# Optimization experiments

Hardware: AMD Instinct MI355X
Metric: run time of the kernel (lower is better)

Reference implementation:

```python
import jax, jax.numpy as jnp
import numpy as np

N_NODES = 50000
N_EDGES = 1600000
N_GRAPHS = 256
IN_CH = 128
HID = 128
OUT_CH = 10


def gcn_conv(x, W, b, src, dst, ew, num_nodes):
    # PyG GCNConv: add self-loops (weight 1), symmetric deg^-1/2 normalization,
    # linear transform first, aggregate via scatter-add, bias after.
    loop = jnp.arange(num_nodes)
    s = jnp.concatenate([src, loop])
    d = jnp.concatenate([dst, loop])
    w = jnp.concatenate([ew, jnp.ones((num_nodes,), x.dtype)])
    deg = jax.ops.segment_sum(w, d, num_segments=num_nodes)
    dinv = jnp.where(deg > 0, jax.lax.rsqrt(deg), 0.0)
    norm = dinv[s] * dinv[d] * w                     # [E+N]
    h = x @ W                                        # [N, H]
    msg = h[s] * norm[:, None]                       # gather + scale
    out = jax.ops.segment_sum(msg, d, num_segments=num_nodes)  # scatter-add
    return out + b


def setup_inputs() -> dict:
    key = jax.random.key(0)
    ks = jax.random.split(key, 12)
    x = jax.random.normal(ks[0], (N_NODES, IN_CH), jnp.float32)
    edge_index = jax.random.randint(ks[1], (2, N_EDGES), 0, N_NODES, jnp.int64)
    edge_weight = jax.random.uniform(ks[2], (N_EDGES,), jnp.float32)
    batch = jnp.sort(jax.random.randint(ks[3], (N_NODES,), 0, N_GRAPHS, jnp.int64))
    s = 1.0 / np.sqrt(HID)
    W1 = jax.random.normal(ks[4], (IN_CH, HID), jnp.float32) / np.sqrt(IN_CH)
    b1 = jnp.zeros((HID,), jnp.float32)
    W2 = jax.random.normal(ks[5], (HID, HID), jnp.float32) * s
    b2 = jnp.zeros((HID,), jnp.float32)
    W3 = jax.random.normal(ks[6], (HID, HID), jnp.float32) * s
    b3 = jnp.zeros((HID,), jnp.float32)
    lw1 = jax.random.normal(ks[7], (HID, HID), jnp.float32) * s
    lb1 = jax.random.normal(ks[8], (HID,), jnp.float32) * s
    lw2 = jax.random.normal(ks[9], (HID, OUT_CH), jnp.float32) * s
    lb2 = jax.random.normal(ks[10], (OUT_CH,), jnp.float32) * s
    return {"x": x, "edge_index": edge_index, "edge_weight": edge_weight,
            "batch": batch, "W1": W1, "b1": b1, "W2": W2, "b2": b2,
            "W3": W3, "b3": b3, "lw1": lw1, "lb1": lb1, "lw2": lw2, "lb2": lb2}


def reference(x, edge_index, edge_weight, batch, W1, b1, W2, b2, W3, b3, lw1, lb1, lw2, lb2):
    src, dst = edge_index[0], edge_index[1]
    h = jax.nn.relu(gcn_conv(x, W1, b1, src, dst, edge_weight, N_NODES))
    h = jax.nn.relu(gcn_conv(h, W2, b2, src, dst, edge_weight, N_NODES))
    h = gcn_conv(h, W3, b3, src, dst, edge_weight, N_NODES)
    # global mean pool over graphs
    sums = jax.ops.segment_sum(h, batch, num_segments=N_GRAPHS)
    cnt = jax.ops.segment_sum(jnp.ones((N_NODES,), h.dtype), batch, num_segments=N_GRAPHS)
    emb = sums / jnp.maximum(cnt, 1.0)[:, None]      # [G, HID]
    out = (emb @ lw1 + lb1) @ lw2 + lb2              # classify: lin1 -> lin2
    return out
```

## Files before the change

### kernel.cpp

```cpp
#include <hip/hip_runtime.h>

#define N_NODES 50000
#define N_EDGES 1600000
#define N_GRAPHS 256
#define HID 128
#define OUT_CH 10
#define NBUCK 512
#define BNODES ((N_NODES + NBUCK - 1) / NBUCK)
#define BCAP 6144
#define P1BLK 250
#define EPB (N_EDGES / P1BLK)
#define DSENTINEL 127
#define NR 4
#define RSTEP ((N_NODES + NR - 1) / NR)
#define PAD_R 40

typedef __bf16 bf16x8 __attribute__((ext_vector_type(8)));
typedef float f32x4 __attribute__((ext_vector_type(4)));

__device__ inline unsigned bf16rne(float f) {
    unsigned u = __float_as_uint(f);
    return (u + 0x7fffu + ((u >> 16) & 1u)) >> 16;
}

__global__ __launch_bounds__(1024) void bucket_k(const int* __restrict__ src,
                                                 const int* __restrict__ dst,
                                                 const float* __restrict__ ew,
                                                 int* __restrict__ bcount,
                                                 int2* __restrict__ cpair) {
    __shared__ int hist[NBUCK];
    __shared__ int base[NBUCK];
    int t = threadIdx.x;
    for (int i = t; i < NBUCK; i += 1024) hist[i] = 0;
    __syncthreads();
    const int ch0 = blockIdx.x * (EPB / 4);
    const int ch1 = ch0 + (EPB / 4);
    const int4* dst4 = (const int4*)dst;
    for (int ci = ch0 + t; ci < ch1; ci += 1024) {
        int4 d4 = dst4[ci];
        atomicAdd(&hist[d4.x / BNODES], 1);
        atomicAdd(&hist[d4.y / BNODES], 1);
        atomicAdd(&hist[d4.z / BNODES], 1);
        atomicAdd(&hist[d4.w / BNODES], 1);
    }
    __syncthreads();
    for (int i = t; i < NBUCK; i += 1024) {
        int c = hist[i];
        base[i] = (c > 0) ? atomicAdd(&bcount[i], (c + 7) & ~7) : 0;
        hist[i] = 0;
    }
    __syncthreads();
    for (int ci = ch0 + t; ci < ch1; ci += 1024) {
        int4 d4 = dst4[ci];
        int e = ci * 4;
#define PROC(dd, ee)                                              \
        {                                                         \
            int b = (dd) / BNODES;                                \
            int off = base[b] + atomicAdd(&hist[b], 1);           \
            if (off < BCAP) {                                     \
                int2 p;                                           \
                p.x = (((dd) - b * BNODES) << 16) | src[ee];      \
                p.y = __float_as_int(ew[ee]);                     \
                cpair[b * BCAP + off] = p;                        \
            }                                                     \
        }
        PROC(d4.x, e)
        PROC(d4.y, e + 1)
        PROC(d4.z, e + 2)
        PROC(d4.w, e + 3)
#undef PROC
    }
    __syncthreads();
    for (int i = t; i < NBUCK; i += 1024) {
        int c = hist[i];
        int ac = (c + 7) & ~7;
        for (int j = c; j < ac; ++j) {
            int off = base[i] + j;
            if (off < BCAP) {
                int2 p;
                p.x = DSENTINEL << 16;
                p.y = 0;
                cpair[i * BCAP + off] = p;
            }
        }
    }
}

__global__ __launch_bounds__(512) void ell_scatter_k(const int* __restrict__ bcount,
                                                     const int2* __restrict__ cpair,
                                                     int2* __restrict__ ell,
                                                     unsigned* __restrict__ fill4,
                                                     float* __restrict__ dinv) {
    __shared__ int lfill[BNODES * NR];
    __shared__ float wsum[BNODES];
    int b = blockIdx.x;
    int t = threadIdx.x;
    for (int i = t; i < BNODES * NR; i += 512) lfill[i] = 0;
    for (int i = t; i < BNODES; i += 512) wsum[i] = 0.f;
    __syncthreads();
    int cnt = bcount[b];
    if (cnt > BCAP) cnt = BCAP;
    int n0 = b * BNODES;
    int sbase = b * BCAP;
    for (int i = t; i < cnt; i += 512) {
        int2 p = cpair[sbase + i];
        int dloc = p.x >> 16;
        if (dloc < BNODES) {
            int s = p.x & 0xffff;
            int r = s / RSTEP;
            int pos = atomicAdd(&lfill[dloc * NR + r], 1);
            atomicAdd(&wsum[dloc], __int_as_float(p.y));
            if (pos < PAD_R) {
                int2 q;
                q.x = s;
                q.y = p.y;
                ell[((size_t)(n0 + dloc) * NR + r) * PAD_R + pos] = q;
            }
        }
    }
    __syncthreads();
    for (int i = t; i < BNODES; i += 512) {
        int n = n0 + i;
        if (n < N_NODES) {
            unsigned f = 0;
#pragma unroll
            for (int r = 0; r < NR; ++r) {
                int c = lfill[i * NR + r];
                if (c > PAD_R) c = PAD_R;
                f |= (unsigned)c << (8 * r);
            }
            fill4[n] = f;
            dinv[n] = rsqrtf(wsum[i] + 1.0f);
        }
    }
}

__global__ __launch_bounds__(256) void prep_k(const int* __restrict__ batch,
                                              int* __restrict__ gstart,
                                              const float* __restrict__ W1,
                                              const float* __restrict__ W2,
                                              const float* __restrict__ W3,
                                              unsigned short* __restrict__ Wt) {
    int idx = blockIdx.x * 256 + threadIdx.x;
    if (idx < 3 * 16384) {
        int m = idx >> 14;
        int r = idx & 16383;
        const float* W = (m == 0) ? W1 : (m == 1) ? W2 : W3;
        int c = r >> 7, k = r & 127;
        Wt[idx] = (unsigned short)bf16rne(W[k * 128 + c]);
    }
    if (idx < N_NODES) {
        int b = batch[idx];
        int bprev = (idx == 0) ? -1 : batch[idx - 1];
        for (int g = bprev + 1; g <= b; ++g) gstart[g] = idx;
        if (idx == N_NODES - 1) {
            for (int g = b + 1; g <= N_GRAPHS; ++g) gstart[g] = N_NODES;
        }
    }
}

__global__ __launch_bounds__(256) void gemm_mfma_k(const float* __restrict__ A32,
                                                   const unsigned short* __restrict__ Ab,
                                                   const unsigned short* __restrict__ Wt,
                                                   unsigned short* __restrict__ Cb,
                                                   int n_rows) {
    int tid = threadIdx.x;
    int wave = tid >> 6;
    int lane = tid & 63;
    int m = lane & 15;
    int quad = lane >> 4;
    int row = blockIdx.x * 64 + wave * 16 + m;
    int rowc = row < n_rows ? row : n_rows - 1;
    f32x4 acc[8] = {};
#pragma unroll
    for (int kc = 0; kc < 4; ++kc) {
        bf16x8 a;
        if (A32) {
            const float4* Ar = (const float4*)(A32 + (size_t)rowc * 128 + kc * 32 + quad * 8);
            float4 lo = Ar[0], hi = Ar[1];
            union { bf16x8 v; unsigned short s[8]; } u;
            u.s[0] = (unsigned short)bf16rne(lo.x);
            u.s[1] = (unsigned short)bf16rne(lo.y);
            u.s[2] = (unsigned short)bf16rne(lo.z);
            u.s[3] = (unsigned short)bf16rne(lo.w);
            u.s[4] = (unsigned short)bf16rne(hi.x);
            u.s[5] = (unsigned short)bf16rne(hi.y);
            u.s[6] = (unsigned short)bf16rne(hi.z);
            u.s[7] = (unsigned short)bf16rne(hi.w);
            a = u.v;
        } else {
            a = *(const bf16x8*)(Ab + (size_t)rowc * 128 + kc * 32 + quad * 8);
        }
#pragma unroll
        for (int ct = 0; ct < 8; ++ct) {
            bf16x8 b = *(const bf16x8*)(Wt + (size_t)(ct * 16 + m) * 128 + kc * 32 + quad * 8);
            acc[ct] = __builtin_amdgcn_mfma_f32_16x16x32_bf16(a, b, acc[ct], 0, 0, 0);
        }
    }
    int obase = blockIdx.x * 64 + wave * 16 + quad * 4;
#pragma unroll
    for (int ct = 0; ct < 8; ++ct) {
#pragma unroll
        for (int r = 0; r < 4; ++r) {
            int n = obase + r;
            if (n < n_rows)
                Cb[(size_t)n * 128 + ct * 16 + m] = (unsigned short)bf16rne(acc[ct][r]);
        }
    }
}

__global__ __launch_bounds__(256) void agg_k(const unsigned short* __restrict__ tb,
                                             const unsigned* __restrict__ fill4,
                                             const int2* __restrict__ ell,
                                             const float* __restrict__ dinv,
                                             const float* __restrict__ bias,
                                             unsigned short* __restrict__ outB, int relu) {
    int lane = threadIdx.x & 15;
    int local = threadIdx.x >> 4;
    int n = blockIdx.x * 16 + local;
    if (n >= N_NODES) return;
    float dn = dinv[n];
#define UNP(q, f)                                                 \
    float f##0 = __uint_as_float((q).x << 16);                    \
    float f##1 = __uint_as_float((q).x & 0xffff0000u);            \
    float f##2 = __uint_as_float((q).y << 16);                    \
    float f##3 = __uint_as_float((q).y & 0xffff0000u);            \
    float f##4 = __uint_as_float((q).z << 16);                    \
    float f##5 = __uint_as_float((q).z & 0xffff0000u);            \
    float f##6 = __uint_as_float((q).w << 16);                    \
    float f##7 = __uint_as_float((q).w & 0xffff0000u);
    uint4 qs = ((const uint4*)(tb + (size_t)n * 128))[lane];
    UNP(qs, s)
    float acc0 = s0 * dn, acc1 = s1 * dn, acc2 = s2 * dn, acc3 = s3 * dn;
    float acc4 = s4 * dn, acc5 = s5 * dn, acc6 = s6 * dn, acc7 = s7 * dn;
    unsigned f4 = fill4[n];
#pragma unroll
    for (int r = 0; r < NR; ++r) {
        int c = (f4 >> (8 * r)) & 255;
        const int2* ep = ell + ((size_t)n * NR + r) * PAD_R;
        int i = 0;
        for (; i + 4 <= c; i += 4) {
            int2 p0 = ep[i], p1 = ep[i + 1], p2 = ep[i + 2], p3 = ep[i + 3];
            uint4 q0 = ((const uint4*)(tb + (size_t)p0.x * 128))[lane];
            uint4 q1 = ((const uint4*)(tb + (size_t)p1.x * 128))[lane];
            uint4 q2 = ((const uint4*)(tb + (size_t)p2.x * 128))[lane];
            uint4 q3 = ((const uint4*)(tb + (size_t)p3.x * 128))[lane];
            float w0 = __int_as_float(p0.y) * dinv[p0.x];
            float w1 = __int_as_float(p1.y) * dinv[p1.x];
            float w2 = __int_as_float(p2.y) * dinv[p2.x];
            float w3 = __int_as_float(p3.y) * dinv[p3.x];
            UNP(q0, a)
            UNP(q1, b)
            UNP(q2, cc)
            UNP(q3, d)
            acc0 += a0 * w0 + b0 * w1 + cc0 * w2 + d0 * w3;
            acc1 += a1 * w0 + b1 * w1 + cc1 * w2 + d1 * w3;
            acc2 += a2 * w0 + b2 * w1 + cc2 * w2 + d2 * w3;
            acc3 += a3 * w0 + b3 * w1 + cc3 * w2 + d3 * w3;
            acc4 += a4 * w0 + b4 * w1 + cc4 * w2 + d4 * w3;
            acc5 += a5 * w0 + b5 * w1 + cc5 * w2 + d5 * w3;
            acc6 += a6 * w0 + b6 * w1 + cc6 * w2 + d6 * w3;
            acc7 += a7 * w0 + b7 * w1 + cc7 * w2 + d7 * w3;
        }
        for (; i < c; ++i) {
            int2 p = ep[i];
            float w = __int_as_float(p.y) * dinv[p.x];
            uint4 q = ((const uint4*)(tb + (size_t)p.x * 128))[lane];
            UNP(q, a)
            acc0 += a0 * w; acc1 += a1 * w; acc2 += a2 * w; acc3 += a3 * w;
            acc4 += a4 * w; acc5 += a5 * w; acc6 += a6 * w; acc7 += a7 * w;
        }
    }
#undef UNP
    float4 b0 = ((const float4*)bias)[lane * 2];
    float4 b1 = ((const float4*)bias)[lane * 2 + 1];
    acc0 = acc0 * dn + b0.x; acc1 = acc1 * dn + b0.y;
    acc2 = acc2 * dn + b0.z; acc3 = acc3 * dn + b0.w;
    acc4 = acc4 * dn + b1.x; acc5 = acc5 * dn + b1.y;
    acc6 = acc6 * dn + b1.z; acc7 = acc7 * dn + b1.w;
    if (relu) {
        acc0 = fmaxf(acc0, 0.f); acc1 = fmaxf(acc1, 0.f);
        acc2 = fmaxf(acc2, 0.f); acc3 = fmaxf(acc3, 0.f);
        acc4 = fmaxf(acc4, 0.f); acc5 = fmaxf(acc5, 0.f);
        acc6 = fmaxf(acc6, 0.f); acc7 = fmaxf(acc7, 0.f);
    }
    uint4 pk;
    pk.x = bf16rne(acc0) | (bf16rne(acc1) << 16);
    pk.y = bf16rne(acc2) | (bf16rne(acc3) << 16);
    pk.z = bf16rne(acc4) | (bf16rne(acc5) << 16);
    pk.w = bf16rne(acc6) | (bf16rne(acc7) << 16);
    ((uint4*)(outB + (size_t)n * 128))[lane] = pk;
}

#define PCHUNK 49
__global__ __launch_bounds__(128) void pool1_k(const unsigned short* __restrict__ hb,
                                               const int* __restrict__ batch,
                                               float* __restrict__ pool) {
    int c = threadIdx.x;
    int n0 = blockIdx.x * PCHUNK;
    if (n0 >= N_NODES) return;
    int n1 = n0 + PCHUNK;
    if (n1 > N_NODES) n1 = N_NODES;
    int g = batch[n0];
    float run = 0.f;
    for (int n = n0; n < n1; ++n) {
        int gn = batch[n];
        if (gn != g) {
            atomicAdd(&pool[g * 128 + c], run);
            run = 0.f;
            g = gn;
        }
        run += __uint_as_float((unsigned)hb[(size_t)n * 128 + c] << 16);
    }
    atomicAdd(&pool[g * 128 + c], run);
}

__global__ __launch_bounds__(128) void cls2_k(const float* __restrict__ pool,
                                              const int* __restrict__ gstart,
                                              const float* __restrict__ lw1,
                                              const float* __restrict__ lb1,
                                              const float* __restrict__ lw2,
                                              const float* __restrict__ lb2,
                                              float* __restrict__ out) {
    __shared__ float emb[128];
    __shared__ float mid[128];
    int g = blockIdx.x, c = threadIdx.x;
    float cntf = fmaxf((float)(gstart[g + 1] - gstart[g]), 1.0f);
    emb[c] = pool[(size_t)g * 128 + c] / cntf;
    __syncthreads();
    float a = lb1[c];
    for (int k = 0; k < 128; ++k) a += emb[k] * lw1[k * 128 + c];
    mid[c] = a;
    __syncthreads();
    if (c < OUT_CH) {
        float o = lb2[c];
        for (int k = 0; k < 128; ++k) o += mid[k] * lw2[k * OUT_CH + c];
        out[g * OUT_CH + c] = o;
    }
}

extern "C" void kernel_launch(void* const* d_in, const int* in_sizes, int n_in,
                              void* d_out, int out_size, void* d_ws, size_t ws_size,
                              hipStream_t stream) {
    const float* x = (const float*)d_in[0];
    const int* ei = (const int*)d_in[1];
    const int* src = ei;
    const int* dst = ei + N_EDGES;
    const float* ew = (const float*)d_in[2];
    const int* batch = (const int*)d_in[3];
    const float* W1 = (const float*)d_in[4];
    const float* b1 = (const float*)d_in[5];
    const float* W2 = (const float*)d_in[6];
    const float* b2 = (const float*)d_in[7];
    const float* W3 = (const float*)d_in[8];
    const float* b3 = (const float*)d_in[9];
    const float* lw1 = (const float*)d_in[10];
    const float* lb1 = (const float*)d_in[11];
    const float* lw2 = (const float*)d_in[12];
    const float* lb2 = (const float*)d_in[13];
    float* out = (float*)d_out;

    char* ws = (char*)d_ws;
    size_t off = 0;
    auto alloc = [&](size_t bytes) {
        size_t cur = off;
        off += (bytes + 255) & ~(size_t)255;
        return cur;
    };
    size_t o_bcount = alloc(NBUCK * 4);
    size_t o_pool = alloc(N_GRAPHS * HID * 4);
    size_t zero_end = off;
    size_t o_fill4 = alloc(N_NODES * 4);
    size_t o_dinv = alloc(N_NODES * 4);
    size_t o_gstart = alloc((N_GRAPHS + 1) * 4);
    size_t o_wt = alloc(3 * 16384 * 2);
    size_t o_ell = alloc((size_t)N_NODES * NR * PAD_R * 8);
    size_t o_cpair = alloc((size_t)NBUCK * BCAP * 8);
    size_t o_gAb = alloc((size_t)N_NODES * HID * 2);
    size_t o_aggB = alloc((size_t)N_NODES * HID * 2);
    (void)ws_size;

    int* bcount = (int*)(ws + o_bcount);
    float* pool = (float*)(ws + o_pool);
    unsigned* fill4 = (unsigned*)(ws + o_fill4);
    float* dinv = (float*)(ws + o_dinv);
    int* gstart = (int*)(ws + o_gstart);
    unsigned short* Wt = (unsigned short*)(ws + o_wt);
    int2* ell = (int2*)(ws + o_ell);
    int2* cpair = (int2*)(ws + o_cpair);
    unsigned short* gAb = (unsigned short*)(ws + o_gAb);
    unsigned short* aggB = (unsigned short*)(ws + o_aggB);

    hipMemsetAsync(d_ws, 0, zero_end, stream);

    bucket_k<<<P1BLK, 1024, 0, stream>>>(src, dst, ew, bcount, cpair);
    ell_scatter_k<<<NBUCK, 512, 0, stream>>>(bcount, cpair, ell, fill4, dinv);
    prep_k<<<196, 256, 0, stream>>>(batch, gstart, W1, W2, W3, Wt);

    int gemm_blocks = (N_NODES + 63) / 64;
    int agg_blocks = (N_NODES + 15) / 16;
    gemm_mfma_k<<<gemm_blocks, 256, 0, stream>>>(x, (const unsigned short*)0, Wt, gAb, N_NODES);
    agg_k<<<agg_blocks, 256, 0, stream>>>(gAb, fill4, ell, dinv, b1, aggB, 1);
    gemm_mfma_k<<<gemm_blocks, 256, 0, stream>>>((const float*)0, aggB, Wt + 16384, gAb, N_NODES);
    agg_k<<<agg_blocks, 256, 0, stream>>>(gAb, fill4, ell, dinv, b2, aggB, 1);
    gemm_mfma_k<<<gemm_blocks, 256, 0, stream>>>((const float*)0, aggB, Wt + 32768, gAb, N_NODES);
    agg_k<<<agg_blocks, 256, 0, stream>>>(gAb, fill4, ell, dinv, b3, aggB, 0);

    pool1_k<<<(N_NODES + PCHUNK - 1) / PCHUNK, 128, 0, stream>>>(aggB, batch, pool);
    cls2_k<<<N_GRAPHS, 128, 0, stream>>>(pool, gstart, lw1, lb1, lw2, lb2, out);
}
```

Measured before the change: 385.7 us.

## Merge four per-range ELL slots into one contiguous row-sorted ELL row

The ELL build now makes two passes per bucket. The first counts edges per source range and sums weights, then per-node prefix offsets are computed so all of a node's edges sit in one contiguous PAD=80 row, still grouped by source range. The aggregation kernel then walks a single list per node, not four short sub-lists, which cuts loop overhead and remainder iterations and lets the 4-way unroll cover more edges. Separately, the bucket kernel loads src and edge weights as vectors. The cost is a second pass over the bucketed pairs, and any node with more than 80 in-edges would be truncated.

Measured after the change: 389.9 us. No clear change (+1.1%).

```diff
diff --git a/kernel.cpp b/kernel.cpp
--- a/kernel.cpp
+++ b/kernel.cpp
@@ -5,6 +5,7 @@
 #define N_GRAPHS 256
 #define HID 128
 #define OUT_CH 10
+#define PAD 80
 #define NBUCK 512
 #define BNODES ((N_NODES + NBUCK - 1) / NBUCK)
 #define BCAP 6144
@@ -13,7 +14,6 @@
 #define DSENTINEL 127
 #define NR 4
 #define RSTEP ((N_NODES + NR - 1) / NR)
-#define PAD_R 40
 
 typedef __bf16 bf16x8 __attribute__((ext_vector_type(8)));
 typedef float f32x4 __attribute__((ext_vector_type(4)));
@@ -36,6 +36,8 @@
     const int ch0 = blockIdx.x * (EPB / 4);
     const int ch1 = ch0 + (EPB / 4);
     const int4* dst4 = (const int4*)dst;
+    const int4* src4 = (const int4*)src;
+    const float4* ew4 = (const float4*)ew;
     for (int ci = ch0 + t; ci < ch1; ci += 1024) {
         int4 d4 = dst4[ci];
         atomicAdd(&hist[d4.x / BNODES], 1);
@@ -52,22 +54,23 @@
     __syncthreads();
     for (int ci = ch0 + t; ci < ch1; ci += 1024) {
         int4 d4 = dst4[ci];
-        int e = ci * 4;
-#define PROC(dd, ee)                                              \
+        int4 s4 = src4[ci];
+        float4 w4 = ew4[ci];
+#define PROC(dd, ss, ww)                                          \
         {                                                         \
             int b = (dd) / BNODES;                                \
             int off = base[b] + atomicAdd(&hist[b], 1);           \
             if (off < BCAP) {                                     \
                 int2 p;                                           \
-                p.x = (((dd) - b * BNODES) << 16) | src[ee];      \
-                p.y = __float_as_int(ew[ee]);                     \
+                p.x = (((dd) - b * BNODES) << 16) | (ss);         \
+                p.y = __float_as_int(ww);                         \
                 cpair[b * BCAP + off] = p;                        \
             }                                                     \
         }
-        PROC(d4.x, e)
-        PROC(d4.y, e + 1)
-        PROC(d4.z, e + 2)
-        PROC(d4.w, e + 3)
+        PROC(d4.x, s4.x, w4.x)
+        PROC(d4.y, s4.y, w4.y)
+        PROC(d4.z, s4.z, w4.z)
+        PROC(d4.w, s4.w, w4.w)
 #undef PROC
     }
     __syncthreads();
@@ -89,13 +92,13 @@
 __global__ __launch_bounds__(512) void ell_scatter_k(const int* __restrict__ bcount,
                                                      const int2* __restrict__ cpair,
                                                      int2* __restrict__ ell,
-                                                     unsigned* __restrict__ fill4,
+                                                     int* __restrict__ fill,
                                                      float* __restrict__ dinv) {
-    __shared__ int lfill[BNODES * NR];
+    __shared__ int lcnt[BNODES * NR];
     __shared__ float wsum[BNODES];
     int b = blockIdx.x;
     int t = threadIdx.x;
-    for (int i = t; i < BNODES * NR; i += 512) lfill[i] = 0;
+    for (int i = t; i < BNODES * NR; i += 512) lcnt[i] = 0;
     for (int i = t; i < BNODES; i += 512) wsum[i] = 0.f;
     __syncthreads();
     int cnt = bcount[b];
@@ -106,31 +109,40 @@
         int2 p = cpair[sbase + i];
         int dloc = p.x >> 16;
         if (dloc < BNODES) {
+            int r = (p.x & 0xffff) / RSTEP;
+            atomicAdd(&lcnt[dloc * NR + r], 1);
+            atomicAdd(&wsum[dloc], __int_as_float(p.y));
+        }
+    }
+    __syncthreads();
+    for (int i = t; i < BNODES; i += 512) {
+        int c0 = lcnt[i * NR + 0], c1 = lcnt[i * NR + 1];
+        int c2 = lcnt[i * NR + 2], c3 = lcnt[i * NR + 3];
+        int total = c0 + c1 + c2 + c3;
+        lcnt[i * NR + 0] = 0;
+        lcnt[i * NR + 1] = c0;
+        lcnt[i * NR + 2] = c0 + c1;
+        lcnt[i * NR + 3] = c0 + c1 + c2;
+        int n = n0 + i;
+        if (n < N_NODES) {
+            fill[n] = total < PAD ? total : PAD;
+            dinv[n] = rsqrtf(wsum[i] + 1.0f);
+        }
+    }
+    __syncthreads();
+    for (int i = t; i < cnt; i += 512) {
+        int2 p = cpair[sbase + i];
+        int dloc = p.x >> 16;
+        if (dloc < BNODES) {
             int s = p.x & 0xffff;
             int r = s / RSTEP;
-            int pos = atomicAdd(&lfill[dloc * NR + r], 1);
-            atomicAdd(&wsum[dloc], __int_as_float(p.y));
-            if (pos < PAD_R) {
+            int pos = atomicAdd(&lcnt[dloc * NR + r], 1);
+            if (pos < PAD) {
                 int2 q;
                 q.x = s;
                 q.y = p.y;
-                ell[((size_t)(n0 + dloc) * NR + r) * PAD_R + pos] = q;
+                ell[(size_t)(n0 + dloc) * PAD + pos] = q;
             }
-        }
-    }
-    __syncthreads();
-    for (int i = t; i < BNODES; i += 512) {
-        int n = n0 + i;
-        if (n < N_NODES) {
-            unsigned f = 0;
-#pragma unroll
-            for (int r = 0; r < NR; ++r) {
-                int c = lfill[i * NR + r];
-                if (c > PAD_R) c = PAD_R;
-                f |= (unsigned)c << (8 * r);
-            }
-            fill4[n] = f;
-            dinv[n] = rsqrtf(wsum[i] + 1.0f);
         }
     }
 }
@@ -210,7 +222,7 @@
 }
 
 __global__ __launch_bounds__(256) void agg_k(const unsigned short* __restrict__ tb,
-                                             const unsigned* __restrict__ fill4,
+                                             const int* __restrict__ fill,
                                              const int2* __restrict__ ell,
                                              const float* __restrict__ dinv,
                                              const float* __restrict__ bias,
@@ -233,43 +245,39 @@
     UNP(qs, s)
     float acc0 = s0 * dn, acc1 = s1 * dn, acc2 = s2 * dn, acc3 = s3 * dn;
     float acc4 = s4 * dn, acc5 = s5 * dn, acc6 = s6 * dn, acc7 = s7 * dn;
-    unsigned f4 = fill4[n];
-#pragma unroll
-    for (int r = 0; r < NR; ++r) {
-        int c = (f4 >> (8 * r)) & 255;
-        const int2* ep = ell + ((size_t)n * NR + r) * PAD_R;
-        int i = 0;
-        for (; i + 4 <= c; i += 4) {
-            int2 p0 = ep[i], p1 = ep[i + 1], p2 = ep[i + 2], p3 = ep[i + 3];
-            uint4 q0 = ((const uint4*)(tb + (size_t)p0.x * 128))[lane];
-            uint4 q1 = ((const uint4*)(tb + (size_t)p1.x * 128))[lane];
-            uint4 q2 = ((const uint4*)(tb + (size_t)p2.x * 128))[lane];
-            uint4 q3 = ((const uint4*)(tb + (size_t)p3.x * 128))[lane];
-            float w0 = __int_as_float(p0.y) * dinv[p0.x];
-            float w1 = __int_as_float(p1.y) * dinv[p1.x];
-            float w2 = __int_as_float(p2.y) * dinv[p2.x];
-            float w3 = __int_as_float(p3.y) * dinv[p3.x];
-            UNP(q0, a)
-            UNP(q1, b)
-            UNP(q2, cc)
-            UNP(q3, d)
-            acc0 += a0 * w0 + b0 * w1 + cc0 * w2 + d0 * w3;
-            acc1 += a1 * w0 + b1 * w1 + cc1 * w2 + d1 * w3;
-            acc2 += a2 * w0 + b2 * w1 + cc2 * w2 + d2 * w3;
-            acc3 += a3 * w0 + b3 * w1 + cc3 * w2 + d3 * w3;
-            acc4 += a4 * w0 + b4 * w1 + cc4 * w2 + d4 * w3;
-            acc5 += a5 * w0 + b5 * w1 + cc5 * w2 + d5 * w3;
-            acc6 += a6 * w0 + b6 * w1 + cc6 * w2 + d6 * w3;
-            acc7 += a7 * w0 + b7 * w1 + cc7 * w2 + d7 * w3;
-        }
-        for (; i < c; ++i) {
-            int2 p = ep[i];
-            float w = __int_as_float(p.y) * dinv[p.x];
-            uint4 q = ((const uint4*)(tb + (size_t)p.x * 128))[lane];
-            UNP(q, a)
-            acc0 += a0 * w; acc1 += a1 * w; acc2 += a2 * w; acc3 += a3 * w;
-            acc4 += a4 * w; acc5 += a5 * w; acc6 += a6 * w; acc7 += a7 * w;
-        }
+    const int2* ep = ell + (size_t)n * PAD;
+    int c = fill[n];
+    int i = 0;
+    for (; i + 4 <= c; i += 4) {
+        int2 p0 = ep[i], p1 = ep[i + 1], p2 = ep[i + 2], p3 = ep[i + 3];
+        uint4 q0 = ((const uint4*)(tb + (size_t)p0.x * 128))[lane];
+        uint4 q1 = ((const uint4*)(tb + (size_t)p1.x * 128))[lane];
+        uint4 q2 = ((const uint4*)(tb + (size_t)p2.x * 128))[lane];
+        uint4 q3 = ((const uint4*)(tb + (size_t)p3.x * 128))[lane];
+        float w0 = __int_as_float(p0.y) * dinv[p0.x];
+        float w1 = __int_as_float(p1.y) * dinv[p1.x];
+        float w2 = __int_as_float(p2.y) * dinv[p2.x];
+        float w3 = __int_as_float(p3.y) * dinv[p3.x];
+        UNP(q0, a)
+        UNP(q1, b)
+        UNP(q2, cc)
+        UNP(q3, d)
+        acc0 += a0 * w0 + b0 * w1 + cc0 * w2 + d0 * w3;
+        acc1 += a1 * w0 + b1 * w1 + cc1 * w2 + d1 * w3;
+        acc2 += a2 * w0 + b2 * w1 + cc2 * w2 + d2 * w3;
+        acc3 += a3 * w0 + b3 * w1 + cc3 * w2 + d3 * w3;
+        acc4 += a4 * w0 + b4 * w1 + cc4 * w2 + d4 * w3;
+        acc5 += a5 * w0 + b5 * w1 + cc5 * w2 + d5 * w3;
+        acc6 += a6 * w0 + b6 * w1 + cc6 * w2 + d6 * w3;
+        acc7 += a7 * w0 + b7 * w1 + cc7 * w2 + d7 * w3;
+    }
+    for (; i < c; ++i) {
+        int2 p = ep[i];
+        float w = __int_as_float(p.y) * dinv[p.x];
+        uint4 q = ((const uint4*)(tb + (size_t)p.x * 128))[lane];
+        UNP(q, a)
+        acc0 += a0 * w; acc1 += a1 * w; acc2 += a2 * w; acc3 += a3 * w;
+        acc4 += a4 * w; acc5 += a5 * w; acc6 += a6 * w; acc7 += a7 * w;
     }
 #undef UNP
     float4 b0 = ((const float4*)bias)[lane * 2];
@@ -370,11 +378,11 @@
     size_t o_bcount = alloc(NBUCK * 4);
     size_t o_pool = alloc(N_GRAPHS * HID * 4);
     size_t zero_end = off;
-    size_t o_fill4 = alloc(N_NODES * 4);
+    size_t o_fill = alloc(N_NODES * 4);
     size_t o_dinv = alloc(N_NODES * 4);
     size_t o_gstart = alloc((N_GRAPHS + 1) * 4);
     size_t o_wt = alloc(3 * 16384 * 2);
-    size_t o_ell = alloc((size_t)N_NODES * NR * PAD_R * 8);
+    size_t o_ell = alloc((size_t)N_NODES * PAD * 8);
     size_t o_cpair = alloc((size_t)NBUCK * BCAP * 8);
     size_t o_gAb = alloc((size_t)N_NODES * HID * 2);
     size_t o_aggB = alloc((size_t)N_NODES * HID * 2);
@@ -382,7 +390,7 @@
 
     int* bcount = (int*)(ws + o_bcount);
     float* pool = (float*)(ws + o_pool);
-    unsigned* fill4 = (unsigned*)(ws + o_fill4);
+    int* fill = (int*)(ws + o_fill);
     float* dinv = (float*)(ws + o_dinv);
     int* gstart = (int*)(ws + o_gstart);
     unsigned short* Wt = (unsigned short*)(ws + o_wt);
@@ -394,17 +402,17 @@
     hipMemsetAsync(d_ws, 0, zero_end, stream);
 
     bucket_k<<<P1BLK, 1024, 0, stream>>>(src, dst, ew, bcount, cpair);
-    ell_scatter_k<<<NBUCK, 512, 0, stream>>>(bcount, cpair, ell, fill4, dinv);
+    ell_scatter_k<<<NBUCK, 512, 0, stream>>>(bcount, cpair, ell, fill, dinv);
     prep_k<<<196, 256, 0, stream>>>(batch, gstart, W1, W2, W3, Wt);
 
     int gemm_blocks = (N_NODES + 63) / 64;
     int agg_blocks = (N_NODES + 15) / 16;
     gemm_mfma_k<<<gemm_blocks, 256, 0, stream>>>(x, (const unsigned short*)0, Wt, gAb, N_NODES);
-    agg_k<<<agg_blocks, 256, 0, stream>>>(gAb, fill4, ell, dinv, b1, aggB, 1);
+    agg_k<<<agg_blocks, 256, 0, stream>>>(gAb, fill, ell, dinv, b1, aggB, 1);
     gemm_mfma_k<<<gemm_blocks, 256, 0, stream>>>((const float*)0, aggB, Wt + 16384, gAb, N_NODES);
-    agg_k<<<agg_blocks, 256, 0, stream>>>(gAb, fill4, ell, dinv, b2, aggB, 1);
+    agg_k<<<agg_blocks, 256, 0, stream>>>(gAb, fill, ell, dinv, b2, aggB, 1);
     gemm_mfma_k<<<gemm_blocks, 256, 0, stream>>>((const float*)0, aggB, Wt + 32768, gAb, N_NODES);
-    agg_k<<<agg_blocks, 256, 0, stream>>>(gAb, fill4, ell, dinv, b3, aggB, 0);
+    agg_k<<<agg_blocks, 256, 0, stream>>>(gAb, fill, ell, dinv, b3, aggB, 0);
 
     pool1_k<<<(N_NODES + PCHUNK - 1) / PCHUNK, 128, 0, stream>>>(aggB, batch, pool);
     cls2_k<<<N_GRAPHS, 128, 0, stream>>>(pool, gstart, lw1, lb1, lw2, lb2, out);
```
